# Performance work log

Hardware: AMD Instinct MI355X
Metric: run time of the kernel (lower is better)

The kernel has to match this reference:

```python
import jax, jax.numpy as jnp
import numpy as np

B, N_PEP, N_REC, EMB, OUT = 4, 4096, 10, 256, 256


def setup_inputs() -> dict:
    key = jax.random.key(0)
    ks = jax.random.split(key, 9)
    s_emb = 1.0 / np.sqrt(EMB)
    s_2emb = 1.0 / np.sqrt(2 * EMB)
    return {
        "rec_node_feat": jax.random.normal(ks[0], (B, N_PEP, N_REC, EMB), jnp.float32),
        "pep_node_feat": jax.random.normal(ks[1], (B, N_PEP, EMB), jnp.float32),
        "edge_feat": jax.random.normal(ks[2], (B, N_PEP, N_REC, EMB), jnp.float32),
        "Wp_w": jax.random.uniform(ks[3], (OUT, EMB), jnp.float32, -s_emb, s_emb),
        "Wp_b": jax.random.uniform(ks[4], (OUT,), jnp.float32, -s_emb, s_emb),
        "Wr_w": jax.random.uniform(ks[5], (OUT, 2 * EMB), jnp.float32, -s_2emb, s_2emb),
        "Wr_b": jax.random.uniform(ks[6], (OUT,), jnp.float32, -s_2emb, s_2emb),
        "Wv_w": jax.random.uniform(ks[7], (OUT, 2 * EMB), jnp.float32, -s_2emb, s_2emb),
        "Wv_b": jax.random.uniform(ks[8], (OUT,), jnp.float32, -s_2emb, s_2emb),
    }


def reference(rec_node_feat, pep_node_feat, edge_feat,
              Wp_w, Wp_b, Wr_w, Wr_b, Wv_w, Wv_b):
    # pep query: [B, N_pep, out]
    pep_query = jnp.einsum('bnd,od->bno', pep_node_feat, Wp_w) + Wp_b
    # receptor + edge concat: [B, N_pep, 10, 2*emb]
    rec_edge = jnp.concatenate((rec_node_feat, edge_feat), axis=3)
    value = jnp.einsum('bnrd,od->bnro', rec_edge, Wv_w) + Wv_b  # [B,N,10,out]
    key_ = jnp.einsum('bnrd,od->bnro', rec_edge, Wr_w) + Wr_b   # [B,N,10,out]
    scale = 1.0 / np.sqrt(OUT).astype(np.float32)
    # elementwise QK dot over out dim -> [B, N, 10]
    logits = jnp.einsum('bno,bnro->bnr', pep_query, key_) * scale
    attention = jax.nn.softmax(logits, axis=2)  # softmax over 10 neighbors
    # weighted value sum + residual projection
    out = pep_query + jnp.einsum('bnr,bnro->bno', attention, value)
    return out
```

## Files before the change

kernel.cpp:

```cpp
#include <hip/hip_runtime.h>
#include <hip/hip_bf16.h>

#define N_TOK   16384
#define NREC    10
#define EMB     256
#define TWO_EMB 512
#define OUTD    256
#define T_BLK   16
#define THREADS 512

typedef __bf16 bf16x8 __attribute__((ext_vector_type(8)));
typedef float  f32x4  __attribute__((ext_vector_type(4)));

static __device__ __forceinline__ unsigned int f2bf_bits(float f) {
    unsigned int u = __builtin_bit_cast(unsigned int, f);
    u = (u + 0x7fffu + ((u >> 16) & 1u)) >> 16;
    return u & 0xffffu;
}
static __device__ __forceinline__ unsigned int pack2(float a, float b) {
    return f2bf_bits(a) | (f2bf_bits(b) << 16);
}
static __device__ __forceinline__ float bflo(unsigned int u) {
    return __builtin_bit_cast(float, u << 16);
}
static __device__ __forceinline__ float bfhi(unsigned int u) {
    return __builtin_bit_cast(float, u & 0xffff0000u);
}

static __device__ __forceinline__ float wave_sum(float p) {
    p += __builtin_bit_cast(float, __builtin_amdgcn_update_dpp(
             0, __builtin_bit_cast(int, p), 0x121, 0xf, 0xf, true));
    p += __builtin_bit_cast(float, __builtin_amdgcn_update_dpp(
             0, __builtin_bit_cast(int, p), 0x122, 0xf, 0xf, true));
    p += __builtin_bit_cast(float, __builtin_amdgcn_update_dpp(
             0, __builtin_bit_cast(int, p), 0x124, 0xf, 0xf, true));
    p += __builtin_bit_cast(float, __builtin_amdgcn_update_dpp(
             0, __builtin_bit_cast(int, p), 0x128, 0xf, 0xf, true));
    p += __shfl_xor(p, 16);
    p += __shfl_xor(p, 32);
    return p;
}

__global__ void prep_wfrag(const float* __restrict__ Wp,
                           const float* __restrict__ Wr,
                           const float* __restrict__ Wv,
                           short* __restrict__ wp_frag,
                           short* __restrict__ wr_frag,
                           short* __restrict__ wv_frag) {
    int idx = blockIdx.x * blockDim.x + threadIdx.x;
    if (idx < 16 * 8 * 64 * 8) {
        int j = idx & 7, lane = (idx >> 3) & 63, kt = (idx >> 9) & 7, nt = idx >> 12;
        int n = nt * 16 + (lane & 15), k = kt * 32 + ((lane >> 4) << 3) + j;
        wp_frag[idx] = (short)f2bf_bits(Wp[n * EMB + k]);
    }
    if (idx < 32 * 8 * 64 * 8) {
        int j = idx & 7, lane = (idx >> 3) & 63, kt = (idx >> 9) & 7, nt = idx >> 12;
        int n = nt * 16 + (lane & 15), k = kt * 32 + ((lane >> 4) << 3) + j;
        wr_frag[idx] = (short)f2bf_bits(Wr[k * TWO_EMB + n]);
    }
    if (idx < 16 * 16 * 64 * 8) {
        int j = idx & 7, lane = (idx >> 3) & 63, kt = (idx >> 9) & 15, nt = idx >> 13;
        int n = nt * 16 + (lane & 15), k = kt * 32 + ((lane >> 4) << 3) + j;
        wv_frag[idx] = (short)f2bf_bits(Wv[n * TWO_EMB + k]);
    }
}

template<int USE_FRAG>
static __device__ __forceinline__ bf16x8 load_b_rm(const short* __restrict__ frag,
                                                   const float* __restrict__ W,
                                                   int n, int k, int ld) {
    if constexpr (USE_FRAG) {
        return *reinterpret_cast<const bf16x8*>(frag);
    } else {
        const float* s = W + (long)n * ld + k;
        float4 f0 = *reinterpret_cast<const float4*>(s);
        float4 f1 = *reinterpret_cast<const float4*>(s + 4);
        uint4 t = { pack2(f0.x, f0.y), pack2(f0.z, f0.w), pack2(f1.x, f1.y), pack2(f1.z, f1.w) };
        return __builtin_bit_cast(bf16x8, t);
    }
}
template<int USE_FRAG>
static __device__ __forceinline__ bf16x8 load_b_tr(const short* __restrict__ frag,
                                                   const float* __restrict__ W,
                                                   int n, int k, int ld) {
    if constexpr (USE_FRAG) {
        return *reinterpret_cast<const bf16x8*>(frag);
    } else {
        unsigned int p[4];
        #pragma unroll
        for (int jj = 0; jj < 4; ++jj)
            p[jj] = pack2(W[(long)(k + 2 * jj) * ld + n], W[(long)(k + 2 * jj + 1) * ld + n]);
        uint4 t = { p[0], p[1], p[2], p[3] };
        return __builtin_bit_cast(bf16x8, t);
    }
}

static __device__ __forceinline__ void stream_token(
    const float* __restrict__ bp,
    const unsigned char* __restrict__ qrb,
    unsigned char* __restrict__ xz,
    int t, int lane,
    float4 s0l, float4 s0h, float4 s1l, float4 s1h,
    float4 s2l, float4 s2h, float4 s3l, float4 s3h)
{
    uint4 qw = *reinterpret_cast<const uint4*>(qrb + t * 1024 + lane * 16);
    const float qa0 = bflo(qw.x), qa1 = bfhi(qw.x), qa2 = bflo(qw.y), qa3 = bfhi(qw.y);
    const float qa4 = bflo(qw.z), qa5 = bfhi(qw.z), qa6 = bflo(qw.w), qa7 = bfhi(qw.w);
    const float C = 0.0625f * 1.4426950408889634f;

    float s = 0.f;
    float4 xb0 = make_float4(0.f, 0.f, 0.f, 0.f), xb1 = xb0;

    #define LD(r, sl, sh) { sl = *reinterpret_cast<const float4*>(bp + (r) * EMB); \
                            sh = *reinterpret_cast<const float4*>(bp + (r) * EMB + 4); }
    #define PROC(sl, sh) { \
        float p = qa0*(sl).x + qa1*(sl).y + qa2*(sl).z + qa3*(sl).w \
                + qa4*(sh).x + qa5*(sh).y + qa6*(sh).z + qa7*(sh).w; \
        p = wave_sum(p); \
        float e = exp2f(p * C);                       \
        s += e; \
        xb0.x += e*(sl).x; xb0.y += e*(sl).y; xb0.z += e*(sl).z; xb0.w += e*(sl).w; \
        xb1.x += e*(sh).x; xb1.y += e*(sh).y; xb1.z += e*(sh).z; xb1.w += e*(sh).w; }

    PROC(s0l, s0h); LD(4, s0l, s0h);
    PROC(s1l, s1h); LD(5, s1l, s1h);
    PROC(s2l, s2h); LD(6, s2l, s2h);
    PROC(s3l, s3h); LD(7, s3l, s3h);
    PROC(s0l, s0h); LD(8, s0l, s0h);
    PROC(s1l, s1h); LD(9, s1l, s1h);
    PROC(s2l, s2h);
    PROC(s3l, s3h);
    PROC(s0l, s0h);
    PROC(s1l, s1h);
    #undef LD
    #undef PROC

    const float inv = 1.f / s;
    uint4 wv4 = { pack2(xb0.x * inv, xb0.y * inv), pack2(xb0.z * inv, xb0.w * inv),
                  pack2(xb1.x * inv, xb1.y * inv), pack2(xb1.z * inv, xb1.w * inv) };
    *reinterpret_cast<uint4*>(xz + 1024 * t + ((lane * 16) ^ ((t & 7) << 4))) = wv4;
}

template<int USE_FRAG>
__launch_bounds__(THREADS, 4)
__global__ void ga9_fused(const float* __restrict__ rec,
                          const float* __restrict__ pep,
                          const float* __restrict__ edge,
                          const float* __restrict__ Wp_w,
                          const float* __restrict__ Wp_b,
                          const float* __restrict__ Wr_w,
                          const float* __restrict__ Wv_w,
                          const float* __restrict__ Wv_b,
                          const short* __restrict__ wp_frag,
                          const short* __restrict__ wr_frag,
                          const short* __restrict__ wv_frag,
                          float* __restrict__ out) {
    __shared__ __align__(16) unsigned char xz[T_BLK * 1024];
    __shared__ __align__(16) unsigned char qbf[T_BLK * 512];
    __shared__ __align__(16) unsigned char qrb[T_BLK * 1024];

    const int tid  = threadIdx.x;
    const int lane = tid & 63;
    const int wave = tid >> 6;
    const int tok0 = blockIdx.x * T_BLK;

    #pragma unroll
    for (int it = 0; it < 2; ++it) {
        int idx = tid + it * THREADS;
        int row = idx >> 6, d4 = (idx & 63) << 2;
        float4 f = *reinterpret_cast<const float4*>(pep + (long)(tok0 + row) * EMB + d4);
        uint2 w = { pack2(f.x, f.y), pack2(f.z, f.w) };
        *reinterpret_cast<uint2*>(xz + 512 * row + ((d4 * 2) ^ ((row & 7) << 4))) = w;
    }
    __syncthreads();

    {
        f32x4 qacc[2] = {};
        #pragma unroll
        for (int kt = 0; kt < 8; ++kt) {
            int kk = kt * 32 + ((lane >> 4) << 3);
            int row = lane & 15;
            bf16x8 a = *reinterpret_cast<const bf16x8*>(xz + 512 * row + ((kk * 2) ^ ((row & 7) << 4)));
            #pragma unroll
            for (int ntl = 0; ntl < 2; ++ntl) {
                int nt = wave * 2 + ntl;
                bf16x8 b = load_b_rm<USE_FRAG>(wp_frag + ((nt * 8 + kt) * 64 + lane) * 8,
                                               Wp_w, nt * 16 + (lane & 15), kk, EMB);
                qacc[ntl] = __builtin_amdgcn_mfma_f32_16x16x32_bf16(a, b, qacc[ntl], 0, 0, 0);
            }
        }
        #pragma unroll
        for (int ntl = 0; ntl < 2; ++ntl) {
            int n = (wave * 2 + ntl) * 16 + (lane & 15);
            float bias = Wp_b[n];
            #pragma unroll
            for (int i = 0; i < 4; ++i) {
                int row = ((lane >> 4) << 2) + i;
                float v = qacc[ntl][i] + bias;
                *reinterpret_cast<unsigned short*>(qbf + 512 * row + ((n * 2) ^ ((row & 7) << 4)))
                    = (unsigned short)f2bf_bits(v);
            }
        }
    }

    const float* srcA = (lane < 32) ? rec : edge;
    const int dloc = (lane * 8) & 255;
    const float* baseA = srcA + (long)(tok0 + wave * 2) * NREC * EMB + dloc;
    const float* baseB = baseA + (long)NREC * EMB;
    float4 a0l = *reinterpret_cast<const float4*>(baseA + 0 * EMB);
    float4 a0h = *reinterpret_cast<const float4*>(baseA + 0 * EMB + 4);
    float4 a1l = *reinterpret_cast<const float4*>(baseA + 1 * EMB);
    float4 a1h = *reinterpret_cast<const float4*>(baseA + 1 * EMB + 4);
    float4 a2l = *reinterpret_cast<const float4*>(baseA + 2 * EMB);
    float4 a2h = *reinterpret_cast<const float4*>(baseA + 2 * EMB + 4);
    float4 a3l = *reinterpret_cast<const float4*>(baseA + 3 * EMB);
    float4 a3h = *reinterpret_cast<const float4*>(baseA + 3 * EMB + 4);
    __syncthreads();

    {
        f32x4 racc[4] = {};
        #pragma unroll
        for (int kt = 0; kt < 8; ++kt) {
            int kk = kt * 32 + ((lane >> 4) << 3);
            int row = lane & 15;
            bf16x8 a = *reinterpret_cast<const bf16x8*>(qbf + 512 * row + ((kk * 2) ^ ((row & 7) << 4)));
            #pragma unroll
            for (int ntl = 0; ntl < 4; ++ntl) {
                int nt = wave * 4 + ntl;
                bf16x8 b = load_b_tr<USE_FRAG>(wr_frag + ((nt * 8 + kt) * 64 + lane) * 8,
                                               Wr_w, nt * 16 + (lane & 15), kk, TWO_EMB);
                racc[ntl] = __builtin_amdgcn_mfma_f32_16x16x32_bf16(a, b, racc[ntl], 0, 0, 0);
            }
        }
        #pragma unroll
        for (int ntl = 0; ntl < 4; ++ntl) {
            int n = (wave * 4 + ntl) * 16 + (lane & 15);
            #pragma unroll
            for (int i = 0; i < 4; ++i) {
                int row = ((lane >> 4) << 2) + i;
                *reinterpret_cast<unsigned short*>(qrb + row * 1024 + n * 2)
                    = (unsigned short)f2bf_bits(racc[ntl][i]);
            }
        }
    }
    __syncthreads();

    stream_token(baseA, qrb, xz, wave * 2, lane, a0l, a0h, a1l, a1h, a2l, a2h, a3l, a3h);
    {
        float4 b0l = *reinterpret_cast<const float4*>(baseB + 0 * EMB);
        float4 b0h = *reinterpret_cast<const float4*>(baseB + 0 * EMB + 4);
        float4 b1l = *reinterpret_cast<const float4*>(baseB + 1 * EMB);
        float4 b1h = *reinterpret_cast<const float4*>(baseB + 1 * EMB + 4);
        float4 b2l = *reinterpret_cast<const float4*>(baseB + 2 * EMB);
        float4 b2h = *reinterpret_cast<const float4*>(baseB + 2 * EMB + 4);
        float4 b3l = *reinterpret_cast<const float4*>(baseB + 3 * EMB);
        float4 b3h = *reinterpret_cast<const float4*>(baseB + 3 * EMB + 4);
        stream_token(baseB, qrb, xz, wave * 2 + 1, lane, b0l, b0h, b1l, b1h, b2l, b2h, b3l, b3h);
    }
    __syncthreads();

    {
        f32x4 oacc[2] = {};
        #pragma unroll
        for (int kt = 0; kt < 16; ++kt) {
            int kk = kt * 32 + ((lane >> 4) << 3);
            int row = lane & 15;
            bf16x8 a = *reinterpret_cast<const bf16x8*>(xz + 1024 * row + ((kk * 2) ^ ((row & 7) << 4)));
            #pragma unroll
            for (int ntl = 0; ntl < 2; ++ntl) {
                int nt = wave * 2 + ntl;
                bf16x8 b = load_b_rm<USE_FRAG>(wv_frag + ((nt * 16 + kt) * 64 + lane) * 8,
                                               Wv_w, nt * 16 + (lane & 15), kk, TWO_EMB);
                oacc[ntl] = __builtin_amdgcn_mfma_f32_16x16x32_bf16(a, b, oacc[ntl], 0, 0, 0);
            }
        }
        #pragma unroll
        for (int ntl = 0; ntl < 2; ++ntl) {
            int n = (wave * 2 + ntl) * 16 + (lane & 15);
            float bv = Wv_b[n];
            #pragma unroll
            for (int i = 0; i < 4; ++i) {
                int row = ((lane >> 4) << 2) + i;
                unsigned short qu = *reinterpret_cast<const unsigned short*>(
                    qbf + 512 * row + ((n * 2) ^ ((row & 7) << 4)));
                float qv = __builtin_bit_cast(float, (unsigned int)qu << 16);
                out[(long)(tok0 + row) * OUTD + n] = qv + oacc[ntl][i] + bv;
            }
        }
    }
}

extern "C" void kernel_launch(void* const* d_in, const int* in_sizes, int n_in,
                              void* d_out, int out_size, void* d_ws, size_t ws_size,
                              hipStream_t stream) {
    const float* rec  = (const float*)d_in[0];
    const float* pep  = (const float*)d_in[1];
    const float* edge = (const float*)d_in[2];
    const float* Wp_w = (const float*)d_in[3];
    const float* Wp_b = (const float*)d_in[4];
    const float* Wr_w = (const float*)d_in[5];
    const float* Wv_w = (const float*)d_in[7];
    const float* Wv_b = (const float*)d_in[8];
    float* out = (float*)d_out;

    const size_t wp_elems = 16 * 8 * 64 * 8;
    const size_t wr_elems = 32 * 8 * 64 * 8;
    const size_t wv_elems = 16 * 16 * 64 * 8;
    const size_t need = (wp_elems + wr_elems + wv_elems) * sizeof(short);
    short* wp_frag = (short*)d_ws;
    short* wr_frag = wp_frag + wp_elems;
    short* wv_frag = wr_frag + wr_elems;

    if (ws_size >= need) {
        prep_wfrag<<<512, 256, 0, stream>>>(Wp_w, Wr_w, Wv_w, wp_frag, wr_frag, wv_frag);
        ga9_fused<1><<<N_TOK / T_BLK, THREADS, 0, stream>>>(rec, pep, edge, Wp_w, Wp_b, Wr_w,
                                                            Wv_w, Wv_b, wp_frag, wr_frag, wv_frag, out);
    } else {
        ga9_fused<0><<<N_TOK / T_BLK, THREADS, 0, stream>>>(rec, pep, edge, Wp_w, Wp_b, Wr_w,
                                                            Wv_w, Wv_b, wp_frag, wr_frag, wv_frag, out);
    }
}
```

Baseline: 95.46 us.

## Fold Wp into Wr key projection and merge query projection into output GEMM

```diff
diff --git a/kernel.cpp b/kernel.cpp
--- a/kernel.cpp
+++ b/kernel.cpp
@@ -41,58 +41,81 @@
     return p;
 }
 
-__global__ void prep_wfrag(const float* __restrict__ Wp,
-                           const float* __restrict__ Wr,
-                           const float* __restrict__ Wv,
-                           short* __restrict__ wp_frag,
-                           short* __restrict__ wr_frag,
-                           short* __restrict__ wv_frag) {
+__global__ void prep_mfrag(const float* __restrict__ Wr,
+                           const float* __restrict__ Wp,
+                           const float* __restrict__ Wp_b,
+                           short* __restrict__ m_frag,
+                           float* __restrict__ c_vec) {
+    __shared__ float WrL[256][16];
+    __shared__ float WpL[256][32];
+    __shared__ float outL[16][32];
+    const int nt = blockIdx.x >> 3, kt = blockIdx.x & 7;
+    const int n0 = nt * 16, k0 = kt * 32;
+    const int t = threadIdx.x;
+    {
+        const float* wr = Wr + t * TWO_EMB + n0;
+        #pragma unroll
+        for (int i = 0; i < 16; ++i) WrL[t][i] = wr[i];
+        const float* wp = Wp + t * EMB + k0;
+        #pragma unroll
+        for (int i = 0; i < 32; ++i) WpL[t][i] = wp[i];
+    }
+    __syncthreads();
+    {
+        int n = t & 15, kl = t >> 4;
+        float acc0 = 0.f, acc1 = 0.f;
+        #pragma unroll 4
+        for (int o = 0; o < 256; ++o) {
+            float w = WrL[o][n];
+            acc0 += w * WpL[o][kl];
+            acc1 += w * WpL[o][kl + 16];
+        }
+        outL[n][kl] = acc0;
+        outL[n][kl + 16] = acc1;
+    }
+    if (kt == 0 && t < 16) {
+        float acc = 0.f;
+        for (int o = 0; o < 256; ++o) acc += WrL[o][t] * Wp_b[o];
+        c_vec[n0 + t] = acc;
+    }
+    __syncthreads();
+    for (int idx = t; idx < 512; idx += 256) {
+        int lane = idx >> 3, j = idx & 7;
+        int n = lane & 15, kl = ((lane >> 4) << 3) + j;
+        m_frag[(((nt * 8 + kt) * 64 + lane) << 3) + j] = (short)f2bf_bits(outL[n][kl]);
+    }
+}
+
+__global__ void prep_wpv(const float* __restrict__ Wp,
+                         const float* __restrict__ Wv,
+                         short* __restrict__ wpv_frag) {
     int idx = blockIdx.x * blockDim.x + threadIdx.x;
-    if (idx < 16 * 8 * 64 * 8) {
-        int j = idx & 7, lane = (idx >> 3) & 63, kt = (idx >> 9) & 7, nt = idx >> 12;
-        int n = nt * 16 + (lane & 15), k = kt * 32 + ((lane >> 4) << 3) + j;
-        wp_frag[idx] = (short)f2bf_bits(Wp[n * EMB + k]);
-    }
-    if (idx < 32 * 8 * 64 * 8) {
-        int j = idx & 7, lane = (idx >> 3) & 63, kt = (idx >> 9) & 7, nt = idx >> 12;
-        int n = nt * 16 + (lane & 15), k = kt * 32 + ((lane >> 4) << 3) + j;
-        wr_frag[idx] = (short)f2bf_bits(Wr[k * TWO_EMB + n]);
-    }
-    if (idx < 16 * 16 * 64 * 8) {
-        int j = idx & 7, lane = (idx >> 3) & 63, kt = (idx >> 9) & 15, nt = idx >> 13;
-        int n = nt * 16 + (lane & 15), k = kt * 32 + ((lane >> 4) << 3) + j;
-        wv_frag[idx] = (short)f2bf_bits(Wv[n * TWO_EMB + k]);
-    }
-}
-
-template<int USE_FRAG>
-static __device__ __forceinline__ bf16x8 load_b_rm(const short* __restrict__ frag,
-                                                   const float* __restrict__ W,
-                                                   int n, int k, int ld) {
-    if constexpr (USE_FRAG) {
-        return *reinterpret_cast<const bf16x8*>(frag);
-    } else {
-        const float* s = W + (long)n * ld + k;
-        float4 f0 = *reinterpret_cast<const float4*>(s);
-        float4 f1 = *reinterpret_cast<const float4*>(s + 4);
-        uint4 t = { pack2(f0.x, f0.y), pack2(f0.z, f0.w), pack2(f1.x, f1.y), pack2(f1.z, f1.w) };
-        return __builtin_bit_cast(bf16x8, t);
-    }
-}
-template<int USE_FRAG>
-static __device__ __forceinline__ bf16x8 load_b_tr(const short* __restrict__ frag,
-                                                   const float* __restrict__ W,
-                                                   int n, int k, int ld) {
-    if constexpr (USE_FRAG) {
-        return *reinterpret_cast<const bf16x8*>(frag);
-    } else {
-        unsigned int p[4];
-        #pragma unroll
-        for (int jj = 0; jj < 4; ++jj)
-            p[jj] = pack2(W[(long)(k + 2 * jj) * ld + n], W[(long)(k + 2 * jj + 1) * ld + n]);
-        uint4 t = { p[0], p[1], p[2], p[3] };
-        return __builtin_bit_cast(bf16x8, t);
-    }
+    if (idx < 16 * 24 * 64 * 8) {
+        int j = idx & 7, lane = (idx >> 3) & 63;
+        int ntkt = idx >> 9, kt = ntkt % 24, nt = ntkt / 24;
+        int n = nt * 16 + (lane & 15);
+        int k = kt * 32 + ((lane >> 4) << 3) + j;
+        float v = (k < 256) ? Wp[n * EMB + k] : Wv[n * TWO_EMB + (k - 256)];
+        wpv_frag[idx] = (short)f2bf_bits(v);
+    }
+}
+
+static __device__ __forceinline__ bf16x8 load_b_rm0(const float* __restrict__ W,
+                                                    int n, int k, int ld) {
+    const float* s = W + (long)n * ld + k;
+    float4 f0 = *reinterpret_cast<const float4*>(s);
+    float4 f1 = *reinterpret_cast<const float4*>(s + 4);
+    uint4 t = { pack2(f0.x, f0.y), pack2(f0.z, f0.w), pack2(f1.x, f1.y), pack2(f1.z, f1.w) };
+    return __builtin_bit_cast(bf16x8, t);
+}
+static __device__ __forceinline__ bf16x8 load_b_tr0(const float* __restrict__ W,
+                                                    int n, int k, int ld) {
+    unsigned int p[4];
+    #pragma unroll
+    for (int jj = 0; jj < 4; ++jj)
+        p[jj] = pack2(W[(long)(k + 2 * jj) * ld + n], W[(long)(k + 2 * jj + 1) * ld + n]);
+    uint4 t = { p[0], p[1], p[2], p[3] };
+    return __builtin_bit_cast(bf16x8, t);
 }
 
 static __device__ __forceinline__ void stream_token(
@@ -141,23 +164,19 @@
     *reinterpret_cast<uint4*>(xz + 1024 * t + ((lane * 16) ^ ((t & 7) << 4))) = wv4;
 }
 
-template<int USE_FRAG>
 __launch_bounds__(THREADS, 4)
-__global__ void ga9_fused(const float* __restrict__ rec,
-                          const float* __restrict__ pep,
-                          const float* __restrict__ edge,
-                          const float* __restrict__ Wp_w,
-                          const float* __restrict__ Wp_b,
-                          const float* __restrict__ Wr_w,
-                          const float* __restrict__ Wv_w,
-                          const float* __restrict__ Wv_b,
-                          const short* __restrict__ wp_frag,
-                          const short* __restrict__ wr_frag,
-                          const short* __restrict__ wv_frag,
-                          float* __restrict__ out) {
+__global__ void ga10_fused(const float* __restrict__ rec,
+                           const float* __restrict__ pep,
+                           const float* __restrict__ edge,
+                           const short* __restrict__ m_frag,
+                           const float* __restrict__ c_vec,
+                           const short* __restrict__ wpv_frag,
+                           const float* __restrict__ Wp_b,
+                           const float* __restrict__ Wv_b,
+                           float* __restrict__ out) {
+    __shared__ __align__(16) unsigned char pepb[T_BLK * 512];
+    __shared__ __align__(16) unsigned char qrb[T_BLK * 1024];
     __shared__ __align__(16) unsigned char xz[T_BLK * 1024];
-    __shared__ __align__(16) unsigned char qbf[T_BLK * 512];
-    __shared__ __align__(16) unsigned char qrb[T_BLK * 1024];
 
     const int tid  = threadIdx.x;
     const int lane = tid & 63;
@@ -170,38 +189,9 @@
         int row = idx >> 6, d4 = (idx & 63) << 2;
         float4 f = *reinterpret_cast<const float4*>(pep + (long)(tok0 + row) * EMB + d4);
         uint2 w = { pack2(f.x, f.y), pack2(f.z, f.w) };
-        *reinterpret_cast<uint2*>(xz + 512 * row + ((d4 * 2) ^ ((row & 7) << 4))) = w;
-    }
-    __syncthreads();
-
-    {
-        f32x4 qacc[2] = {};
-        #pragma unroll
-        for (int kt = 0; kt < 8; ++kt) {
-            int kk = kt * 32 + ((lane >> 4) << 3);
-            int row = lane & 15;
-            bf16x8 a = *reinterpret_cast<const bf16x8*>(xz + 512 * row + ((kk * 2) ^ ((row & 7) << 4)));
-            #pragma unroll
-            for (int ntl = 0; ntl < 2; ++ntl) {
-                int nt = wave * 2 + ntl;
-                bf16x8 b = load_b_rm<USE_FRAG>(wp_frag + ((nt * 8 + kt) * 64 + lane) * 8,
-                                               Wp_w, nt * 16 + (lane & 15), kk, EMB);
-                qacc[ntl] = __builtin_amdgcn_mfma_f32_16x16x32_bf16(a, b, qacc[ntl], 0, 0, 0);
-            }
-        }
-        #pragma unroll
-        for (int ntl = 0; ntl < 2; ++ntl) {
-            int n = (wave * 2 + ntl) * 16 + (lane & 15);
-            float bias = Wp_b[n];
-            #pragma unroll
-            for (int i = 0; i < 4; ++i) {
-                int row = ((lane >> 4) << 2) + i;
-                float v = qacc[ntl][i] + bias;
-                *reinterpret_cast<unsigned short*>(qbf + 512 * row + ((n * 2) ^ ((row & 7) << 4)))
-                    = (unsigned short)f2bf_bits(v);
-            }
-        }
-    }
+        *reinterpret_cast<uint2*>(pepb + 512 * row + ((d4 * 2) ^ ((row & 7) << 4))) = w;
+    }
+    __syncthreads();
 
     const float* srcA = (lane < 32) ? rec : edge;
     const int dloc = (lane * 8) & 255;
@@ -215,7 +205,6 @@
     float4 a2h = *reinterpret_cast<const float4*>(baseA + 2 * EMB + 4);
     float4 a3l = *reinterpret_cast<const float4*>(baseA + 3 * EMB);
     float4 a3h = *reinterpret_cast<const float4*>(baseA + 3 * EMB + 4);
-    __syncthreads();
 
     {
         f32x4 racc[4] = {};
@@ -223,23 +212,23 @@
         for (int kt = 0; kt < 8; ++kt) {
             int kk = kt * 32 + ((lane >> 4) << 3);
             int row = lane & 15;
-            bf16x8 a = *reinterpret_cast<const bf16x8*>(qbf + 512 * row + ((kk * 2) ^ ((row & 7) << 4)));
+            bf16x8 a = *reinterpret_cast<const bf16x8*>(pepb + 512 * row + ((kk * 2) ^ ((row & 7) << 4)));
             #pragma unroll
             for (int ntl = 0; ntl < 4; ++ntl) {
                 int nt = wave * 4 + ntl;
-                bf16x8 b = load_b_tr<USE_FRAG>(wr_frag + ((nt * 8 + kt) * 64 + lane) * 8,
-                                               Wr_w, nt * 16 + (lane & 15), kk, TWO_EMB);
+                bf16x8 b = *reinterpret_cast<const bf16x8*>(m_frag + (((nt * 8 + kt) * 64 + lane) << 3));
                 racc[ntl] = __builtin_amdgcn_mfma_f32_16x16x32_bf16(a, b, racc[ntl], 0, 0, 0);
             }
         }
         #pragma unroll
         for (int ntl = 0; ntl < 4; ++ntl) {
             int n = (wave * 4 + ntl) * 16 + (lane & 15);
+            float cv = c_vec[n];
             #pragma unroll
             for (int i = 0; i < 4; ++i) {
                 int row = ((lane >> 4) << 2) + i;
                 *reinterpret_cast<unsigned short*>(qrb + row * 1024 + n * 2)
-                    = (unsigned short)f2bf_bits(racc[ntl][i]);
+                    = (unsigned short)f2bf_bits(racc[ntl][i] + cv);
             }
         }
     }
@@ -262,6 +251,150 @@
     {
         f32x4 oacc[2] = {};
         #pragma unroll
+        for (int kt = 0; kt < 24; ++kt) {
+            int row = lane & 15;
+            bf16x8 a;
+            if (kt < 8) {
+                int kk = kt * 32 + ((lane >> 4) << 3);
+                a = *reinterpret_cast<const bf16x8*>(pepb + 512 * row + ((kk * 2) ^ ((row & 7) << 4)));
+            } else {
+                int kk = (kt - 8) * 32 + ((lane >> 4) << 3);
+                a = *reinterpret_cast<const bf16x8*>(xz + 1024 * row + ((kk * 2) ^ ((row & 7) << 4)));
+            }
+            #pragma unroll
+            for (int ntl = 0; ntl < 2; ++ntl) {
+                int nt = wave * 2 + ntl;
+                bf16x8 b = *reinterpret_cast<const bf16x8*>(wpv_frag + (((nt * 24 + kt) * 64 + lane) << 3));
+                oacc[ntl] = __builtin_amdgcn_mfma_f32_16x16x32_bf16(a, b, oacc[ntl], 0, 0, 0);
+            }
+        }
+        #pragma unroll
+        for (int ntl = 0; ntl < 2; ++ntl) {
+            int n = (wave * 2 + ntl) * 16 + (lane & 15);
+            float bias = Wp_b[n] + Wv_b[n];
+            #pragma unroll
+            for (int i = 0; i < 4; ++i) {
+                int row = ((lane >> 4) << 2) + i;
+                out[(long)(tok0 + row) * OUTD + n] = oacc[ntl][i] + bias;
+            }
+        }
+    }
+}
+
+__launch_bounds__(THREADS, 4)
+__global__ void ga_fb(const float* __restrict__ rec,
+                      const float* __restrict__ pep,
+                      const float* __restrict__ edge,
+                      const float* __restrict__ Wp_w,
+                      const float* __restrict__ Wp_b,
+                      const float* __restrict__ Wr_w,
+                      const float* __restrict__ Wv_w,
+                      const float* __restrict__ Wv_b,
+                      float* __restrict__ out) {
+    __shared__ __align__(16) unsigned char xz[T_BLK * 1024];
+    __shared__ __align__(16) unsigned char qbf[T_BLK * 512];
+    __shared__ __align__(16) unsigned char qrb[T_BLK * 1024];
+
+    const int tid  = threadIdx.x;
+    const int lane = tid & 63;
+    const int wave = tid >> 6;
+    const int tok0 = blockIdx.x * T_BLK;
+
+    #pragma unroll
+    for (int it = 0; it < 2; ++it) {
+        int idx = tid + it * THREADS;
+        int row = idx >> 6, d4 = (idx & 63) << 2;
+        float4 f = *reinterpret_cast<const float4*>(pep + (long)(tok0 + row) * EMB + d4);
+        uint2 w = { pack2(f.x, f.y), pack2(f.z, f.w) };
+        *reinterpret_cast<uint2*>(xz + 512 * row + ((d4 * 2) ^ ((row & 7) << 4))) = w;
+    }
+    __syncthreads();
+
+    {
+        f32x4 qacc[2] = {};
+        #pragma unroll
+        for (int kt = 0; kt < 8; ++kt) {
+            int kk = kt * 32 + ((lane >> 4) << 3);
+            int row = lane & 15;
+            bf16x8 a = *reinterpret_cast<const bf16x8*>(xz + 512 * row + ((kk * 2) ^ ((row & 7) << 4)));
+            #pragma unroll
+            for (int ntl = 0; ntl < 2; ++ntl) {
+                int nt = wave * 2 + ntl;
+                bf16x8 b = load_b_rm0(Wp_w, nt * 16 + (lane & 15), kk, EMB);
+                qacc[ntl] = __builtin_amdgcn_mfma_f32_16x16x32_bf16(a, b, qacc[ntl], 0, 0, 0);
+            }
+        }
+        #pragma unroll
+        for (int ntl = 0; ntl < 2; ++ntl) {
+            int n = (wave * 2 + ntl) * 16 + (lane & 15);
+            float bias = Wp_b[n];
+            #pragma unroll
+            for (int i = 0; i < 4; ++i) {
+                int row = ((lane >> 4) << 2) + i;
+                *reinterpret_cast<unsigned short*>(qbf + 512 * row + ((n * 2) ^ ((row & 7) << 4)))
+                    = (unsigned short)f2bf_bits(qacc[ntl][i] + bias);
+            }
+        }
+    }
+
+    const float* srcA = (lane < 32) ? rec : edge;
+    const int dloc = (lane * 8) & 255;
+    const float* baseA = srcA + (long)(tok0 + wave * 2) * NREC * EMB + dloc;
+    const float* baseB = baseA + (long)NREC * EMB;
+    float4 a0l = *reinterpret_cast<const float4*>(baseA + 0 * EMB);
+    float4 a0h = *reinterpret_cast<const float4*>(baseA + 0 * EMB + 4);
+    float4 a1l = *reinterpret_cast<const float4*>(baseA + 1 * EMB);
+    float4 a1h = *reinterpret_cast<const float4*>(baseA + 1 * EMB + 4);
+    float4 a2l = *reinterpret_cast<const float4*>(baseA + 2 * EMB);
+    float4 a2h = *reinterpret_cast<const float4*>(baseA + 2 * EMB + 4);
+    float4 a3l = *reinterpret_cast<const float4*>(baseA + 3 * EMB);
+    float4 a3h = *reinterpret_cast<const float4*>(baseA + 3 * EMB + 4);
+    __syncthreads();
+
+    {
+        f32x4 racc[4] = {};
+        #pragma unroll
+        for (int kt = 0; kt < 8; ++kt) {
+            int kk = kt * 32 + ((lane >> 4) << 3);
+            int row = lane & 15;
+            bf16x8 a = *reinterpret_cast<const bf16x8*>(qbf + 512 * row + ((kk * 2) ^ ((row & 7) << 4)));
+            #pragma unroll
+            for (int ntl = 0; ntl < 4; ++ntl) {
+                int nt = wave * 4 + ntl;
+                bf16x8 b = load_b_tr0(Wr_w, nt * 16 + (lane & 15), kk, TWO_EMB);
+                racc[ntl] = __builtin_amdgcn_mfma_f32_16x16x32_bf16(a, b, racc[ntl], 0, 0, 0);
+            }
+        }
+        #pragma unroll
+        for (int ntl = 0; ntl < 4; ++ntl) {
+            int n = (wave * 4 + ntl) * 16 + (lane & 15);
+            #pragma unroll
+            for (int i = 0; i < 4; ++i) {
+                int row = ((lane >> 4) << 2) + i;
+                *reinterpret_cast<unsigned short*>(qrb + row * 1024 + n * 2)
+                    = (unsigned short)f2bf_bits(racc[ntl][i]);
+            }
+        }
+    }
+    __syncthreads();
+
+    stream_token(baseA, qrb, xz, wave * 2, lane, a0l, a0h, a1l, a1h, a2l, a2h, a3l, a3h);
+    {
+        float4 b0l = *reinterpret_cast<const float4*>(baseB + 0 * EMB);
+        float4 b0h = *reinterpret_cast<const float4*>(baseB + 0 * EMB + 4);
+        float4 b1l = *reinterpret_cast<const float4*>(baseB + 1 * EMB);
+        float4 b1h = *reinterpret_cast<const float4*>(baseB + 1 * EMB + 4);
+        float4 b2l = *reinterpret_cast<const float4*>(baseB + 2 * EMB);
+        float4 b2h = *reinterpret_cast<const float4*>(baseB + 2 * EMB + 4);
+        float4 b3l = *reinterpret_cast<const float4*>(baseB + 3 * EMB);
+        float4 b3h = *reinterpret_cast<const float4*>(baseB + 3 * EMB + 4);
+        stream_token(baseB, qrb, xz, wave * 2 + 1, lane, b0l, b0h, b1l, b1h, b2l, b2h, b3l, b3h);
+    }
+    __syncthreads();
+
+    {
+        f32x4 oacc[2] = {};
+        #pragma unroll
         for (int kt = 0; kt < 16; ++kt) {
             int kk = kt * 32 + ((lane >> 4) << 3);
             int row = lane & 15;
@@ -269,8 +402,7 @@
             #pragma unroll
             for (int ntl = 0; ntl < 2; ++ntl) {
                 int nt = wave * 2 + ntl;
-                bf16x8 b = load_b_rm<USE_FRAG>(wv_frag + ((nt * 16 + kt) * 64 + lane) * 8,
-                                               Wv_w, nt * 16 + (lane & 15), kk, TWO_EMB);
+                bf16x8 b = load_b_rm0(Wv_w, nt * 16 + (lane & 15), kk, TWO_EMB);
                 oacc[ntl] = __builtin_amdgcn_mfma_f32_16x16x32_bf16(a, b, oacc[ntl], 0, 0, 0);
             }
         }
@@ -303,20 +435,20 @@
     const float* Wv_b = (const float*)d_in[8];
     float* out = (float*)d_out;
 
-    const size_t wp_elems = 16 * 8 * 64 * 8;
-    const size_t wr_elems = 32 * 8 * 64 * 8;
-    const size_t wv_elems = 16 * 16 * 64 * 8;
-    const size_t need = (wp_elems + wr_elems + wv_elems) * sizeof(short);
-    short* wp_frag = (short*)d_ws;
-    short* wr_frag = wp_frag + wp_elems;
-    short* wv_frag = wr_frag + wr_elems;
+    const size_t m_elems   = 32 * 8 * 64 * 8;
+    const size_t wpv_elems = 16 * 24 * 64 * 8;
+    const size_t need = (m_elems + wpv_elems) * sizeof(short) + 512 * sizeof(float);
+    short* m_frag   = (short*)d_ws;
+    short* wpv_frag = m_frag + m_elems;
+    float* c_vec    = (float*)(wpv_frag + wpv_elems);
 
     if (ws_size >= need) {
-        prep_wfrag<<<512, 256, 0, stream>>>(Wp_w, Wr_w, Wv_w, wp_frag, wr_frag, wv_frag);
-        ga9_fused<1><<<N_TOK / T_BLK, THREADS, 0, stream>>>(rec, pep, edge, Wp_w, Wp_b, Wr_w,
-                                                            Wv_w, Wv_b, wp_frag, wr_frag, wv_frag, out);
+        prep_mfrag<<<256, 256, 0, stream>>>(Wr_w, Wp_w, Wp_b, m_frag, c_vec);
+        prep_wpv<<<768, 256, 0, stream>>>(Wp_w, Wv_w, wpv_frag);
+        ga10_fused<<<N_TOK / T_BLK, THREADS, 0, stream>>>(rec, pep, edge, m_frag, c_vec,
+                                                          wpv_frag, Wp_b, Wv_b, out);
     } else {
-        ga9_fused<0><<<N_TOK / T_BLK, THREADS, 0, stream>>>(rec, pep, edge, Wp_w, Wp_b, Wr_w,
-                                                            Wv_w, Wv_b, wp_frag, wr_frag, wv_frag, out);
-    }
-}
+        ga_fb<<<N_TOK / T_BLK, THREADS, 0, stream>>>(rec, pep, edge, Wp_w, Wp_b, Wr_w,
+                                                     Wv_w, Wv_b, out);
+    }
+}
```

After: 106.6 us. +11.7%, slower.

## Double tokens per block to reuse weight fragments across two M-tiles

Applied to the files above, without the earlier changes.

```diff
diff --git a/kernel.cpp b/kernel.cpp
--- a/kernel.cpp
+++ b/kernel.cpp
@@ -6,7 +6,7 @@
 #define EMB     256
 #define TWO_EMB 512
 #define OUTD    256
-#define T_BLK   16
+#define T_BLK   32
 #define THREADS 512
 
 typedef __bf16 bf16x8 __attribute__((ext_vector_type(8)));
@@ -65,45 +65,33 @@
     }
 }
 
-template<int USE_FRAG>
-static __device__ __forceinline__ bf16x8 load_b_rm(const short* __restrict__ frag,
-                                                   const float* __restrict__ W,
-                                                   int n, int k, int ld) {
-    if constexpr (USE_FRAG) {
-        return *reinterpret_cast<const bf16x8*>(frag);
-    } else {
-        const float* s = W + (long)n * ld + k;
-        float4 f0 = *reinterpret_cast<const float4*>(s);
-        float4 f1 = *reinterpret_cast<const float4*>(s + 4);
-        uint4 t = { pack2(f0.x, f0.y), pack2(f0.z, f0.w), pack2(f1.x, f1.y), pack2(f1.z, f1.w) };
-        return __builtin_bit_cast(bf16x8, t);
-    }
-}
-template<int USE_FRAG>
-static __device__ __forceinline__ bf16x8 load_b_tr(const short* __restrict__ frag,
-                                                   const float* __restrict__ W,
-                                                   int n, int k, int ld) {
-    if constexpr (USE_FRAG) {
-        return *reinterpret_cast<const bf16x8*>(frag);
-    } else {
-        unsigned int p[4];
-        #pragma unroll
-        for (int jj = 0; jj < 4; ++jj)
-            p[jj] = pack2(W[(long)(k + 2 * jj) * ld + n], W[(long)(k + 2 * jj + 1) * ld + n]);
-        uint4 t = { p[0], p[1], p[2], p[3] };
-        return __builtin_bit_cast(bf16x8, t);
-    }
+static __device__ __forceinline__ bf16x8 load_b_rm0(const float* __restrict__ W,
+                                                    int n, int k, int ld) {
+    const float* s = W + (long)n * ld + k;
+    float4 f0 = *reinterpret_cast<const float4*>(s);
+    float4 f1 = *reinterpret_cast<const float4*>(s + 4);
+    uint4 t = { pack2(f0.x, f0.y), pack2(f0.z, f0.w), pack2(f1.x, f1.y), pack2(f1.z, f1.w) };
+    return __builtin_bit_cast(bf16x8, t);
+}
+static __device__ __forceinline__ bf16x8 load_b_tr0(const float* __restrict__ W,
+                                                    int n, int k, int ld) {
+    unsigned int p[4];
+    #pragma unroll
+    for (int jj = 0; jj < 4; ++jj)
+        p[jj] = pack2(W[(long)(k + 2 * jj) * ld + n], W[(long)(k + 2 * jj + 1) * ld + n]);
+    uint4 t = { p[0], p[1], p[2], p[3] };
+    return __builtin_bit_cast(bf16x8, t);
 }
 
 static __device__ __forceinline__ void stream_token(
     const float* __restrict__ bp,
-    const unsigned char* __restrict__ qrb,
-    unsigned char* __restrict__ xz,
+    const unsigned char* __restrict__ qr_in,
+    unsigned char* __restrict__ xz_out,
     int t, int lane,
     float4 s0l, float4 s0h, float4 s1l, float4 s1h,
     float4 s2l, float4 s2h, float4 s3l, float4 s3h)
 {
-    uint4 qw = *reinterpret_cast<const uint4*>(qrb + t * 1024 + lane * 16);
+    uint4 qw = *reinterpret_cast<const uint4*>(qr_in + t * 1024 + lane * 16);
     const float qa0 = bflo(qw.x), qa1 = bfhi(qw.x), qa2 = bflo(qw.y), qa3 = bfhi(qw.y);
     const float qa4 = bflo(qw.z), qa5 = bfhi(qw.z), qa6 = bflo(qw.w), qa7 = bfhi(qw.w);
     const float C = 0.0625f * 1.4426950408889634f;
@@ -138,26 +126,26 @@
     const float inv = 1.f / s;
     uint4 wv4 = { pack2(xb0.x * inv, xb0.y * inv), pack2(xb0.z * inv, xb0.w * inv),
                   pack2(xb1.x * inv, xb1.y * inv), pack2(xb1.z * inv, xb1.w * inv) };
-    *reinterpret_cast<uint4*>(xz + 1024 * t + ((lane * 16) ^ ((t & 7) << 4))) = wv4;
+    *reinterpret_cast<uint4*>(xz_out + 1024 * t + ((lane * 16) ^ ((t & 7) << 4))) = wv4;
 }
 
 template<int USE_FRAG>
 __launch_bounds__(THREADS, 4)
-__global__ void ga9_fused(const float* __restrict__ rec,
-                          const float* __restrict__ pep,
-                          const float* __restrict__ edge,
-                          const float* __restrict__ Wp_w,
-                          const float* __restrict__ Wp_b,
-                          const float* __restrict__ Wr_w,
-                          const float* __restrict__ Wv_w,
-                          const float* __restrict__ Wv_b,
-                          const short* __restrict__ wp_frag,
-                          const short* __restrict__ wr_frag,
-                          const short* __restrict__ wv_frag,
-                          float* __restrict__ out) {
-    __shared__ __align__(16) unsigned char xz[T_BLK * 1024];
+__global__ void ga11_fused(const float* __restrict__ rec,
+                           const float* __restrict__ pep,
+                           const float* __restrict__ edge,
+                           const float* __restrict__ Wp_w,
+                           const float* __restrict__ Wp_b,
+                           const float* __restrict__ Wr_w,
+                           const float* __restrict__ Wv_w,
+                           const float* __restrict__ Wv_b,
+                           const short* __restrict__ wp_frag,
+                           const short* __restrict__ wr_frag,
+                           const short* __restrict__ wv_frag,
+                           float* __restrict__ out) {
+    __shared__ __align__(16) unsigned char pepb[T_BLK * 512];
     __shared__ __align__(16) unsigned char qbf[T_BLK * 512];
-    __shared__ __align__(16) unsigned char qrb[T_BLK * 1024];
+    __shared__ __align__(16) unsigned char qrx[T_BLK * 1024];
 
     const int tid  = threadIdx.x;
     const int lane = tid & 63;
@@ -165,126 +153,147 @@
     const int tok0 = blockIdx.x * T_BLK;
 
     #pragma unroll
-    for (int it = 0; it < 2; ++it) {
+    for (int it = 0; it < 4; ++it) {
         int idx = tid + it * THREADS;
         int row = idx >> 6, d4 = (idx & 63) << 2;
         float4 f = *reinterpret_cast<const float4*>(pep + (long)(tok0 + row) * EMB + d4);
         uint2 w = { pack2(f.x, f.y), pack2(f.z, f.w) };
-        *reinterpret_cast<uint2*>(xz + 512 * row + ((d4 * 2) ^ ((row & 7) << 4))) = w;
+        *reinterpret_cast<uint2*>(pepb + 512 * row + ((d4 * 2) ^ ((row & 7) << 4))) = w;
     }
     __syncthreads();
 
     {
-        f32x4 qacc[2] = {};
+        f32x4 qacc[2][2] = {};
         #pragma unroll
         for (int kt = 0; kt < 8; ++kt) {
             int kk = kt * 32 + ((lane >> 4) << 3);
-            int row = lane & 15;
-            bf16x8 a = *reinterpret_cast<const bf16x8*>(xz + 512 * row + ((kk * 2) ^ ((row & 7) << 4)));
+            int r0 = lane & 15, r1 = 16 + r0;
+            bf16x8 a0 = *reinterpret_cast<const bf16x8*>(pepb + 512 * r0 + ((kk * 2) ^ ((r0 & 7) << 4)));
+            bf16x8 a1 = *reinterpret_cast<const bf16x8*>(pepb + 512 * r1 + ((kk * 2) ^ ((r1 & 7) << 4)));
             #pragma unroll
             for (int ntl = 0; ntl < 2; ++ntl) {
                 int nt = wave * 2 + ntl;
-                bf16x8 b = load_b_rm<USE_FRAG>(wp_frag + ((nt * 8 + kt) * 64 + lane) * 8,
-                                               Wp_w, nt * 16 + (lane & 15), kk, EMB);
-                qacc[ntl] = __builtin_amdgcn_mfma_f32_16x16x32_bf16(a, b, qacc[ntl], 0, 0, 0);
-            }
-        }
-        #pragma unroll
-        for (int ntl = 0; ntl < 2; ++ntl) {
-            int n = (wave * 2 + ntl) * 16 + (lane & 15);
-            float bias = Wp_b[n];
-            #pragma unroll
-            for (int i = 0; i < 4; ++i) {
-                int row = ((lane >> 4) << 2) + i;
-                float v = qacc[ntl][i] + bias;
-                *reinterpret_cast<unsigned short*>(qbf + 512 * row + ((n * 2) ^ ((row & 7) << 4)))
-                    = (unsigned short)f2bf_bits(v);
+                bf16x8 b;
+                if constexpr (USE_FRAG) b = *reinterpret_cast<const bf16x8*>(wp_frag + (((nt * 8 + kt) * 64 + lane) << 3));
+                else                    b = load_b_rm0(Wp_w, nt * 16 + (lane & 15), kk, EMB);
+                qacc[0][ntl] = __builtin_amdgcn_mfma_f32_16x16x32_bf16(a0, b, qacc[0][ntl], 0, 0, 0);
+                qacc[1][ntl] = __builtin_amdgcn_mfma_f32_16x16x32_bf16(a1, b, qacc[1][ntl], 0, 0, 0);
+            }
+        }
+        #pragma unroll
+        for (int mt = 0; mt < 2; ++mt) {
+            #pragma unroll
+            for (int ntl = 0; ntl < 2; ++ntl) {
+                int n = (wave * 2 + ntl) * 16 + (lane & 15);
+                float bias = Wp_b[n];
+                #pragma unroll
+                for (int i = 0; i < 4; ++i) {
+                    int row = mt * 16 + ((lane >> 4) << 2) + i;
+                    *reinterpret_cast<unsigned short*>(qbf + 512 * row + ((n * 2) ^ ((row & 7) << 4)))
+                        = (unsigned short)f2bf_bits(qacc[mt][ntl][i] + bias);
+                }
             }
         }
     }
 
     const float* srcA = (lane < 32) ? rec : edge;
     const int dloc = (lane * 8) & 255;
-    const float* baseA = srcA + (long)(tok0 + wave * 2) * NREC * EMB + dloc;
-    const float* baseB = baseA + (long)NREC * EMB;
-    float4 a0l = *reinterpret_cast<const float4*>(baseA + 0 * EMB);
-    float4 a0h = *reinterpret_cast<const float4*>(baseA + 0 * EMB + 4);
-    float4 a1l = *reinterpret_cast<const float4*>(baseA + 1 * EMB);
-    float4 a1h = *reinterpret_cast<const float4*>(baseA + 1 * EMB + 4);
-    float4 a2l = *reinterpret_cast<const float4*>(baseA + 2 * EMB);
-    float4 a2h = *reinterpret_cast<const float4*>(baseA + 2 * EMB + 4);
-    float4 a3l = *reinterpret_cast<const float4*>(baseA + 3 * EMB);
-    float4 a3h = *reinterpret_cast<const float4*>(baseA + 3 * EMB + 4);
+    const float* base0 = srcA + (long)(tok0 + wave * 4) * NREC * EMB + dloc;
+    float4 a0l = *reinterpret_cast<const float4*>(base0 + 0 * EMB);
+    float4 a0h = *reinterpret_cast<const float4*>(base0 + 0 * EMB + 4);
+    float4 a1l = *reinterpret_cast<const float4*>(base0 + 1 * EMB);
+    float4 a1h = *reinterpret_cast<const float4*>(base0 + 1 * EMB + 4);
+    float4 a2l = *reinterpret_cast<const float4*>(base0 + 2 * EMB);
+    float4 a2h = *reinterpret_cast<const float4*>(base0 + 2 * EMB + 4);
+    float4 a3l = *reinterpret_cast<const float4*>(base0 + 3 * EMB);
+    float4 a3h = *reinterpret_cast<const float4*>(base0 + 3 * EMB + 4);
     __syncthreads();
 
     {
-        f32x4 racc[4] = {};
+        f32x4 racc[2][4] = {};
         #pragma unroll
         for (int kt = 0; kt < 8; ++kt) {
             int kk = kt * 32 + ((lane >> 4) << 3);
-            int row = lane & 15;
-            bf16x8 a = *reinterpret_cast<const bf16x8*>(qbf + 512 * row + ((kk * 2) ^ ((row & 7) << 4)));
+            int r0 = lane & 15, r1 = 16 + r0;
+            bf16x8 a0 = *reinterpret_cast<const bf16x8*>(qbf + 512 * r0 + ((kk * 2) ^ ((r0 & 7) << 4)));
+            bf16x8 a1 = *reinterpret_cast<const bf16x8*>(qbf + 512 * r1 + ((kk * 2) ^ ((r1 & 7) << 4)));
             #pragma unroll
             for (int ntl = 0; ntl < 4; ++ntl) {
                 int nt = wave * 4 + ntl;
-                bf16x8 b = load_b_tr<USE_FRAG>(wr_frag + ((nt * 8 + kt) * 64 + lane) * 8,
-                                               Wr_w, nt * 16 + (lane & 15), kk, TWO_EMB);
-                racc[ntl] = __builtin_amdgcn_mfma_f32_16x16x32_bf16(a, b, racc[ntl], 0, 0, 0);
-            }
-        }
-        #pragma unroll
-        for (int ntl = 0; ntl < 4; ++ntl) {
-            int n = (wave * 4 + ntl) * 16 + (lane & 15);
-            #pragma unroll
-            for (int i = 0; i < 4; ++i) {
-                int row = ((lane >> 4) << 2) + i;
-                *reinterpret_cast<unsigned short*>(qrb + row * 1024 + n * 2)
-                    = (unsigned short)f2bf_bits(racc[ntl][i]);
+                bf16x8 b;
+                if constexpr (USE_FRAG) b = *reinterpret_cast<const bf16x8*>(wr_frag + (((nt * 8 + kt) * 64 + lane) << 3));
+                else                    b = load_b_tr0(Wr_w, nt * 16 + (lane & 15), kk, TWO_EMB);
+                racc[0][ntl] = __builtin_amdgcn_mfma_f32_16x16x32_bf16(a0, b, racc[0][ntl], 0, 0, 0);
+                racc[1][ntl] = __builtin_amdgcn_mfma_f32_16x16x32_bf16(a1, b, racc[1][ntl], 0, 0, 0);
+            }
+        }
+        #pragma unroll
+        for (int mt = 0; mt < 2; ++mt) {
+            #pragma unroll
+            for (int ntl = 0; ntl < 4; ++ntl) {
+                int n = (wave * 4 + ntl) * 16 + (lane & 15);
+                #pragma unroll
+                for (int i = 0; i < 4; ++i) {
+                    int row = mt * 16 + ((lane >> 4) << 2) + i;
+                    *reinterpret_cast<unsigned short*>(qrx + row * 1024 + n * 2)
+                        = (unsigned short)f2bf_bits(racc[mt][ntl][i]);
+                }
             }
         }
     }
     __syncthreads();
 
-    stream_token(baseA, qrb, xz, wave * 2, lane, a0l, a0h, a1l, a1h, a2l, a2h, a3l, a3h);
     {
-        float4 b0l = *reinterpret_cast<const float4*>(baseB + 0 * EMB);
-        float4 b0h = *reinterpret_cast<const float4*>(baseB + 0 * EMB + 4);
-        float4 b1l = *reinterpret_cast<const float4*>(baseB + 1 * EMB);
-        float4 b1h = *reinterpret_cast<const float4*>(baseB + 1 * EMB + 4);
-        float4 b2l = *reinterpret_cast<const float4*>(baseB + 2 * EMB);
-        float4 b2h = *reinterpret_cast<const float4*>(baseB + 2 * EMB + 4);
-        float4 b3l = *reinterpret_cast<const float4*>(baseB + 3 * EMB);
-        float4 b3h = *reinterpret_cast<const float4*>(baseB + 3 * EMB + 4);
-        stream_token(baseB, qrb, xz, wave * 2 + 1, lane, b0l, b0h, b1l, b1h, b2l, b2h, b3l, b3h);
+        const int t0 = wave * 4;
+        stream_token(base0, qrx, qrx, t0, lane, a0l, a0h, a1l, a1h, a2l, a2h, a3l, a3h);
+        #pragma unroll
+        for (int k = 1; k < 4; ++k) {
+            const float* bp = base0 + (long)k * NREC * EMB;
+            float4 b0l = *reinterpret_cast<const float4*>(bp + 0 * EMB);
+            float4 b0h = *reinterpret_cast<const float4*>(bp + 0 * EMB + 4);
+            float4 b1l = *reinterpret_cast<const float4*>(bp + 1 * EMB);
+            float4 b1h = *reinterpret_cast<const float4*>(bp + 1 * EMB + 4);
+            float4 b2l = *reinterpret_cast<const float4*>(bp + 2 * EMB);
+            float4 b2h = *reinterpret_cast<const float4*>(bp + 2 * EMB + 4);
+            float4 b3l = *reinterpret_cast<const float4*>(bp + 3 * EMB);
+            float4 b3h = *reinterpret_cast<const float4*>(bp + 3 * EMB + 4);
+            stream_token(bp, qrx, qrx, t0 + k, lane, b0l, b0h, b1l, b1h, b2l, b2h, b3l, b3h);
+        }
     }
     __syncthreads();
 
     {
-        f32x4 oacc[2] = {};
+        f32x4 oacc[2][2] = {};
         #pragma unroll
         for (int kt = 0; kt < 16; ++kt) {
             int kk = kt * 32 + ((lane >> 4) << 3);
-            int row = lane & 15;
-            bf16x8 a = *reinterpret_cast<const bf16x8*>(xz + 1024 * row + ((kk * 2) ^ ((row & 7) << 4)));
+            int r0 = lane & 15, r1 = 16 + r0;
+            bf16x8 a0 = *reinterpret_cast<const bf16x8*>(qrx + 1024 * r0 + ((kk * 2) ^ ((r0 & 7) << 4)));
+            bf16x8 a1 = *reinterpret_cast<const bf16x8*>(qrx + 1024 * r1 + ((kk * 2) ^ ((r1 & 7) << 4)));
             #pragma unroll
             for (int ntl = 0; ntl < 2; ++ntl) {
                 int nt = wave * 2 + ntl;
-                bf16x8 b = load_b_rm<USE_FRAG>(wv_frag + ((nt * 16 + kt) * 64 + lane) * 8,
-                                               Wv_w, nt * 16 + (lane & 15), kk, TWO_EMB);
-                oacc[ntl] = __builtin_amdgcn_mfma_f32_16x16x32_bf16(a, b, oacc[ntl], 0, 0, 0);
-            }
-        }
-        #pragma unroll
-        for (int ntl = 0; ntl < 2; ++ntl) {
-            int n = (wave * 2 + ntl) * 16 + (lane & 15);
-            float bv = Wv_b[n];
-            #pragma unroll
-            for (int i = 0; i < 4; ++i) {
-                int row = ((lane >> 4) << 2) + i;
-                unsigned short qu = *reinterpret_cast<const unsigned short*>(
-                    qbf + 512 * row + ((n * 2) ^ ((row & 7) << 4)));
-                float qv = __builtin_bit_cast(float, (unsigned int)qu << 16);
-                out[(long)(tok0 + row) * OUTD + n] = qv + oacc[ntl][i] + bv;
+                bf16x8 b;
+                if constexpr (USE_FRAG) b = *reinterpret_cast<const bf16x8*>(wv_frag + (((nt * 16 + kt) * 64 + lane) << 3));
+                else                    b = load_b_rm0(Wv_w, nt * 16 + (lane & 15), kk, TWO_EMB);
+                oacc[0][ntl] = __builtin_amdgcn_mfma_f32_16x16x32_bf16(a0, b, oacc[0][ntl], 0, 0, 0);
+                oacc[1][ntl] = __builtin_amdgcn_mfma_f32_16x16x32_bf16(a1, b, oacc[1][ntl], 0, 0, 0);
+            }
+        }
+        #pragma unroll
+        for (int mt = 0; mt < 2; ++mt) {
+            #pragma unroll
+            for (int ntl = 0; ntl < 2; ++ntl) {
+                int n = (wave * 2 + ntl) * 16 + (lane & 15);
+                float bv = Wv_b[n];
+                #pragma unroll
+                for (int i = 0; i < 4; ++i) {
+                    int row = mt * 16 + ((lane >> 4) << 2) + i;
+                    unsigned short qu = *reinterpret_cast<const unsigned short*>(
+                        qbf + 512 * row + ((n * 2) ^ ((row & 7) << 4)));
+                    float qv = __builtin_bit_cast(float, (unsigned int)qu << 16);
+                    out[(long)(tok0 + row) * OUTD + n] = qv + oacc[mt][ntl][i] + bv;
+                }
             }
         }
     }
@@ -313,10 +322,10 @@
 
     if (ws_size >= need) {
         prep_wfrag<<<512, 256, 0, stream>>>(Wp_w, Wr_w, Wv_w, wp_frag, wr_frag, wv_frag);
-        ga9_fused<1><<<N_TOK / T_BLK, THREADS, 0, stream>>>(rec, pep, edge, Wp_w, Wp_b, Wr_w,
-                                                            Wv_w, Wv_b, wp_frag, wr_frag, wv_frag, out);
+        ga11_fused<1><<<N_TOK / T_BLK, THREADS, 0, stream>>>(rec, pep, edge, Wp_w, Wp_b, Wr_w,
+                                                             Wv_w, Wv_b, wp_frag, wr_frag, wv_frag, out);
     } else {
-        ga9_fused<0><<<N_TOK / T_BLK, THREADS, 0, stream>>>(rec, pep, edge, Wp_w, Wp_b, Wr_w,
-                                                            Wv_w, Wv_b, wp_frag, wr_frag, wv_frag, out);
-    }
-}
+        ga11_fused<0><<<N_TOK / T_BLK, THREADS, 0, stream>>>(rec, pep, edge, Wp_w, Wp_b, Wr_w,
+                                                             Wv_w, Wv_b, wp_frag, wr_frag, wv_frag, out);
+    }
+}
```

After: 102.0 us. 1.07x slower.
